# Kernel tuning notes

Hardware: AMD Instinct MI355X
Metric: run time of the kernel (lower is better)

## Reference

```python
import jax, jax.numpy as jnp
import numpy as np

B, N, D = 8, 2048, 512

def setup_inputs() -> dict:
    key = jax.random.key(0)
    k1, k2, k3, k4 = jax.random.split(key, 4)
    x = jax.random.normal(k1, (B, N, D), dtype=jnp.float32)
    x2 = jax.random.normal(k2, (B, N, D), dtype=jnp.float32)
    # nn.Linear(dim, dim): weight [D, D], bias [D]
    W = jax.random.normal(k3, (D, D), dtype=jnp.float32) * (1.0 / np.sqrt(D))
    b = jax.random.normal(k4, (D,), dtype=jnp.float32) * 0.01
    return {"x": x, "x2": x2, "W": W, "b": b}

def reference(x, x2, W, b):
    # key = softmax(x2.transpose(1,2), dim=1) -> softmax over feature axis D,
    # shape [B, D, N]; equivalently softmax(x2, axis=-1) then transpose.
    key_t = jax.nn.softmax(x2, axis=-1)          # [B, N, D], softmax over D
    query = jax.nn.softmax(x2, axis=1)            # [B, N, D], softmax over N
    # context = value @ key : [B,N,D] @ [B,D,N] -> [B,N,N]
    context = jnp.einsum('bnd,bmd->bnm', x, key_t)
    # atten = context @ query : [B,N,N] @ [B,N,D] -> [B,N,D]
    atten = jnp.einsum('bnm,bmd->bnd', context, query)
    # linear projection: atten @ W.T + b
    return jnp.einsum('bnd,ed->bne', atten, W) + b
```

## Files before the change

### kernel.cpp

```cpp
#include <hip/hip_runtime.h>


typedef __attribute__((ext_vector_type(8))) short          s16x8;
typedef __attribute__((ext_vector_type(8))) unsigned short u16x8;
typedef __attribute__((ext_vector_type(4))) float          f32x4;

#define B_ 8
#define N_ 2048
#define D_ 512

__device__ inline unsigned short f2bf(float f) {
    unsigned u = __float_as_uint(f);
    u += 0x7FFFu + ((u >> 16) & 1u);
    return (unsigned short)(u >> 16);
}

__global__ __launch_bounds__(256) void fused_sums_k(const float* __restrict__ x2,
                                                    float* __restrict__ rks,
                                                    float* __restrict__ qs) {
    __shared__ float cp[4][512];
    int w = threadIdx.x >> 6, l = threadIdx.x & 63;
    int rbase = blockIdx.x * 32;
    int b = rbase / N_;
    const int c0 = l * 8;
    float colacc[8] = {0.f, 0.f, 0.f, 0.f, 0.f, 0.f, 0.f, 0.f};
#pragma unroll
    for (int rr = 0; rr < 8; ++rr) {
        int r = rbase + w * 8 + rr;
        const float* p = x2 + (size_t)r * D_ + c0;
        float4 a = *(const float4*)p;
        float4 bb = *(const float4*)(p + 4);
        float e0 = __expf(a.x), e1 = __expf(a.y), e2 = __expf(a.z), e3 = __expf(a.w);
        float e4 = __expf(bb.x), e5 = __expf(bb.y), e6 = __expf(bb.z), e7 = __expf(bb.w);
        float s = e0 + e1 + e2 + e3 + e4 + e5 + e6 + e7;
#pragma unroll
        for (int off = 1; off < 64; off <<= 1) s += __shfl_xor(s, off);
        if (l == 0) rks[r] = 1.0f / s;
        colacc[0] += e0; colacc[1] += e1; colacc[2] += e2; colacc[3] += e3;
        colacc[4] += e4; colacc[5] += e5; colacc[6] += e6; colacc[7] += e7;
    }
#pragma unroll
    for (int c = 0; c < 8; ++c) cp[w][c0 + c] = colacc[c];
    __syncthreads();
    for (int c = threadIdx.x; c < 512; c += 256) {
        float s = cp[0][c] + cp[1][c] + cp[2][c] + cp[3][c];
        atomicAdd(&qs[b * D_ + c], s);
    }
}

__global__ __launch_bounds__(256) void softmax_tr_k(const float* __restrict__ x2,
                                                    const float* __restrict__ rks,
                                                    const float* __restrict__ qs,
                                                    unsigned short* __restrict__ Kt,
                                                    unsigned short* __restrict__ Qt) {
    __shared__ unsigned short kt[64][65], qt[64][65];
    int b = blockIdx.z, d0 = blockIdx.y * 64, m0 = blockIdx.x * 64;
    int tx = threadIdx.x & 63, w = threadIdx.x >> 6;
    float rq = 1.0f / qs[b * D_ + d0 + tx];
#pragma unroll
    for (int it = 0; it < 16; ++it) {
        int row = w * 16 + it;
        float v = x2[((size_t)b * N_ + m0 + row) * D_ + d0 + tx];
        float e = __expf(v);
        float rk = rks[b * N_ + m0 + row];
        kt[tx][row] = f2bf(e * rk);
        qt[tx][row] = f2bf(e * rq);
    }
    __syncthreads();
#pragma unroll
    for (int it = 0; it < 16; ++it) {
        int dr = w * 16 + it;
        size_t off = ((size_t)b * D_ + d0 + dr) * N_ + m0 + tx;
        Kt[off] = kt[dr][tx];
        Qt[off] = qt[dr][tx];
    }
}

__global__ __launch_bounds__(256) void cvt_bf16_k(const float* __restrict__ in,
                                                  unsigned short* __restrict__ out) {
    size_t i = ((size_t)blockIdx.x * 256 + threadIdx.x) * 8;
    float4 a = *(const float4*)(in + i);
    float4 b = *(const float4*)(in + i + 4);
    u16x8 o;
    o[0] = f2bf(a.x); o[1] = f2bf(a.y); o[2] = f2bf(a.z); o[3] = f2bf(a.w);
    o[4] = f2bf(b.x); o[5] = f2bf(b.y); o[6] = f2bf(b.z); o[7] = f2bf(b.w);
    *(u16x8*)(out + i) = o;
}

__device__ inline void gload16(const unsigned short* g, unsigned short* l) {
    __builtin_amdgcn_global_load_lds((const __attribute__((address_space(1))) void*)g,
                                     (__attribute__((address_space(3))) void*)l, 16, 0, 0);
}

template <int MODE>
__global__ __launch_bounds__(256, 4) void gemm64_k(const unsigned short* __restrict__ A,
                                                   const unsigned short* __restrict__ Bm,
                                                   void* __restrict__ Cv,
                                                   int M, int N, int K, int nsplit,
                                                   long long sA, long long sB, long long sC) {
    __shared__ unsigned short As[64 * 32], Bs[64 * 32];
    int b = blockIdx.z / nsplit, ks = blockIdx.z % nsplit;
    int klen = K / nsplit, k0 = ks * klen;
    const unsigned short* Ab = A + (size_t)b * sA;
    const unsigned short* Bb = Bm + (size_t)b * sB;
    int tid = threadIdx.x, w = tid >> 6, l = tid & 63;
    int wr = w >> 1, wc = w & 1;
    int lr = l & 15, lg = l >> 4;
    int srow = tid >> 2, scc = tid & 3;

    f32x4 acc[2][2];
#pragma unroll
    for (int i = 0; i < 2; ++i)
#pragma unroll
        for (int j = 0; j < 2; ++j) acc[i][j] = (f32x4){0.f, 0.f, 0.f, 0.f};

    const int rowbase = blockIdx.y * 64, colbase = blockIdx.x * 64;

    for (int kt = k0; kt < k0 + klen; kt += 32) {
        gload16(Ab + (size_t)(rowbase + srow) * K + kt + scc * 8, As + w * 512);
        gload16(Bb + (size_t)(colbase + srow) * K + kt + scc * 8, Bs + w * 512);
        __syncthreads();
        s16x8 af[2], bf[2];
#pragma unroll
        for (int i = 0; i < 2; ++i)
            af[i] = *(const s16x8*)&As[(wr * 32 + i * 16 + lr) * 32 + lg * 8];
#pragma unroll
        for (int j = 0; j < 2; ++j)
            bf[j] = *(const s16x8*)&Bs[(wc * 32 + j * 16 + lr) * 32 + lg * 8];
#pragma unroll
        for (int i = 0; i < 2; ++i)
#pragma unroll
            for (int j = 0; j < 2; ++j)
                acc[i][j] = __builtin_amdgcn_mfma_f32_16x16x32_bf16(af[i], bf[j], acc[i][j], 0, 0, 0);
        __syncthreads();
    }

    if (MODE == 0) {
        float* C = (float*)Cv + (size_t)b * sC;
#pragma unroll
        for (int i = 0; i < 2; ++i)
#pragma unroll
            for (int j = 0; j < 2; ++j) {
                int col = colbase + wc * 32 + j * 16 + lr;
#pragma unroll
                for (int r = 0; r < 4; ++r) {
                    int row = rowbase + wr * 32 + i * 16 + lg * 4 + r;
                    atomicAdd(&C[(size_t)row * N + col], acc[i][j][r]);
                }
            }
    } else {
        unsigned short* C = (unsigned short*)Cv + (size_t)b * sC;
#pragma unroll
        for (int i = 0; i < 2; ++i)
#pragma unroll
            for (int j = 0; j < 2; ++j) {
                int col = colbase + wc * 32 + j * 16 + lr;
#pragma unroll
                for (int r = 0; r < 4; ++r) {
                    int row = rowbase + wr * 32 + i * 16 + lg * 4 + r;
                    C[(size_t)row * N + col] = f2bf(acc[i][j][r]);
                }
            }
    }
}

__global__ __launch_bounds__(256, 2) void gemm_bt_k(const unsigned short* __restrict__ A,
                                                    const unsigned short* __restrict__ Bm,
                                                    float* __restrict__ Cv,
                                                    const float* __restrict__ bias,
                                                    int M, int N, int K,
                                                    long long sA, long long sB, long long sC) {
    __shared__ unsigned short As[128 * 32], Bs[128 * 32];
    int b = blockIdx.z;
    const unsigned short* Ab = A + (size_t)b * sA;
    const unsigned short* Bb = Bm + (size_t)b * sB;
    int tm = blockIdx.y, tn = blockIdx.x;
    int tid = threadIdx.x, w = tid >> 6, l = tid & 63;
    int wr = w >> 1, wc = w & 1;
    int lr = l & 15, lg = l >> 4;

    f32x4 acc[4][4];
#pragma unroll
    for (int i = 0; i < 4; ++i)
#pragma unroll
        for (int j = 0; j < 4; ++j) acc[i][j] = (f32x4){0.f, 0.f, 0.f, 0.f};

    const int rowbase = tm * 128, colbase = tn * 128;

    for (int kt = 0; kt < K; kt += 32) {
#pragma unroll
        for (int i = 0; i < 2; ++i) {
            int ci = (i * 4 + w) * 64 + l;
            int row = ci >> 2, cc = ci & 3;
            gload16(Ab + (size_t)(rowbase + row) * K + kt + cc * 8, As + (i * 4 + w) * 512);
            gload16(Bb + (size_t)(colbase + row) * K + kt + cc * 8, Bs + (i * 4 + w) * 512);
        }
        __syncthreads();
        s16x8 af[4], bf[4];
#pragma unroll
        for (int i = 0; i < 4; ++i)
            af[i] = *(const s16x8*)&As[(wr * 64 + i * 16 + lr) * 32 + lg * 8];
#pragma unroll
        for (int j = 0; j < 4; ++j)
            bf[j] = *(const s16x8*)&Bs[(wc * 64 + j * 16 + lr) * 32 + lg * 8];
#pragma unroll
        for (int i = 0; i < 4; ++i)
#pragma unroll
            for (int j = 0; j < 4; ++j)
                acc[i][j] = __builtin_amdgcn_mfma_f32_16x16x32_bf16(af[i], bf[j], acc[i][j], 0, 0, 0);
        __syncthreads();
    }

    float* C = Cv + (size_t)b * sC;
#pragma unroll
    for (int i = 0; i < 4; ++i)
#pragma unroll
        for (int j = 0; j < 4; ++j) {
            int col = colbase + wc * 64 + j * 16 + lr;
            float bv = bias[col];
#pragma unroll
            for (int r = 0; r < 4; ++r) {
                int row = rowbase + wr * 64 + i * 16 + lg * 4 + r;
                C[(size_t)row * N + col] = acc[i][j][r] + bv;
            }
        }
}

extern "C" void kernel_launch(void* const* d_in, const int* in_sizes, int n_in,
                              void* d_out, int out_size, void* d_ws, size_t ws_size,
                              hipStream_t stream) {
    const float* x    = (const float*)d_in[0];
    const float* x2   = (const float*)d_in[1];
    const float* W    = (const float*)d_in[2];
    const float* bias = (const float*)d_in[3];
    float* out = (float*)d_out;

    unsigned short* Kt  = (unsigned short*)d_ws;
    unsigned short* Qt  = Kt + 8388608;
    unsigned short* xb  = Qt + 8388608;
    unsigned short* Wb  = xb + 8388608;
    unsigned short* KQb = Wb + 262144;
    unsigned short* Mt  = KQb + 2097152;
    float* KQf = (float*)(Mt + 2097152);
    float* qs  = KQf + 2097152;
    float* rks = qs + 4096;

    hipMemsetAsync(KQf, 0, (2097152 + 4096) * sizeof(float), stream);

    fused_sums_k<<<dim3(B_ * N_ / 32), 256, 0, stream>>>(x2, rks, qs);

    softmax_tr_k<<<dim3(N_ / 64, D_ / 64, B_), 256, 0, stream>>>(x2, rks, qs, Kt, Qt);

    cvt_bf16_k<<<dim3(4096), 256, 0, stream>>>(x, xb);
    cvt_bf16_k<<<dim3(128), 256, 0, stream>>>(W, Wb);

    gemm64_k<0><<<dim3(8, 8, B_ * 2), 256, 0, stream>>>(
        Kt, Qt, KQf, 512, 512, 2048, 2,
        (long long)512 * 2048, (long long)512 * 2048, (long long)512 * 512);

    cvt_bf16_k<<<dim3(1024), 256, 0, stream>>>(KQf, KQb);

    gemm64_k<2><<<dim3(8, 8, B_), 256, 0, stream>>>(
        Wb, KQb, Mt, 512, 512, 512, 1,
        0LL, (long long)512 * 512, (long long)512 * 512);

    gemm_bt_k<<<dim3(4, 16, B_), 256, 0, stream>>>(
        xb, Mt, out, bias, 2048, 512, 512,
        (long long)2048 * 512, (long long)512 * 512, (long long)2048 * 512);
}
```

Baseline: 193.5 us.

## Factor softmax scales into one shared transposed matrix and fuse x conversion into GEMM

The row-softmax factor (split as sqrt of 1/rowsum) and the column-softmax denominator are factored out, so a single transposed bf16 matrix F serves both sides of the K^T Q GEMM. The column normalisation moves into the conversion kernel that also sums the two split-K partials. This replaces the atomic adds and the large memset. The final GEMM now loads fp32 x straight into LDS and converts it to bf16 in registers, which removes the separate x conversion pass. The changes halve the transposed write traffic and remove a full pass over x, at the cost of doubled LDS for the A tile and per-iteration conversion work in the last GEMM.

Measured after the change: 183.1 us. -5.4%, faster.

```diff
diff --git a/kernel.cpp b/kernel.cpp
--- a/kernel.cpp
+++ b/kernel.cpp
@@ -16,7 +16,7 @@
 }
 
 __global__ __launch_bounds__(256) void fused_sums_k(const float* __restrict__ x2,
-                                                    float* __restrict__ rks,
+                                                    float* __restrict__ rsq,
                                                     float* __restrict__ qs) {
     __shared__ float cp[4][512];
     int w = threadIdx.x >> 6, l = threadIdx.x & 63;
@@ -35,7 +35,7 @@
         float s = e0 + e1 + e2 + e3 + e4 + e5 + e6 + e7;
 #pragma unroll
         for (int off = 1; off < 64; off <<= 1) s += __shfl_xor(s, off);
-        if (l == 0) rks[r] = 1.0f / s;
+        if (l == 0) rsq[r] = sqrtf(1.0f / s);
         colacc[0] += e0; colacc[1] += e1; colacc[2] += e2; colacc[3] += e3;
         colacc[4] += e4; colacc[5] += e5; colacc[6] += e6; colacc[7] += e7;
     }
@@ -48,31 +48,26 @@
     }
 }
 
-__global__ __launch_bounds__(256) void softmax_tr_k(const float* __restrict__ x2,
-                                                    const float* __restrict__ rks,
-                                                    const float* __restrict__ qs,
-                                                    unsigned short* __restrict__ Kt,
-                                                    unsigned short* __restrict__ Qt) {
-    __shared__ unsigned short kt[64][65], qt[64][65];
-    int b = blockIdx.z, d0 = blockIdx.y * 64, m0 = blockIdx.x * 64;
+__global__ __launch_bounds__(256) void softmax_ft_k(const float* __restrict__ x2,
+                                                    const float* __restrict__ rsq,
+                                                    unsigned short* __restrict__ Ft) {
+    __shared__ unsigned short ft[64][65];
+    int b  = 7 - blockIdx.z;
+    int d0 = (7 - blockIdx.y) * 64;
+    int m0 = (31 - blockIdx.x) * 64;
     int tx = threadIdx.x & 63, w = threadIdx.x >> 6;
-    float rq = 1.0f / qs[b * D_ + d0 + tx];
 #pragma unroll
     for (int it = 0; it < 16; ++it) {
         int row = w * 16 + it;
         float v = x2[((size_t)b * N_ + m0 + row) * D_ + d0 + tx];
-        float e = __expf(v);
-        float rk = rks[b * N_ + m0 + row];
-        kt[tx][row] = f2bf(e * rk);
-        qt[tx][row] = f2bf(e * rq);
+        float sc = rsq[b * N_ + m0 + row];
+        ft[tx][row] = f2bf(__expf(v) * sc);
     }
     __syncthreads();
 #pragma unroll
     for (int it = 0; it < 16; ++it) {
         int dr = w * 16 + it;
-        size_t off = ((size_t)b * D_ + d0 + dr) * N_ + m0 + tx;
-        Kt[off] = kt[dr][tx];
-        Qt[off] = qt[dr][tx];
+        Ft[((size_t)b * D_ + d0 + dr) * N_ + m0 + tx] = ft[dr][tx];
     }
 }
 
@@ -87,7 +82,32 @@
     *(u16x8*)(out + i) = o;
 }
 
+__global__ __launch_bounds__(256) void cvt_kq_k(const float* __restrict__ P,
+                                                const float* __restrict__ qs,
+                                                unsigned short* __restrict__ KQb) {
+    size_t o = ((size_t)blockIdx.x * 256 + threadIdx.x) * 8;
+    int b = (int)(o >> 18);
+    size_t off = o & 262143;
+    int j0 = (int)(o & 511);
+    const float* p0 = P + ((size_t)b * 2) * 262144 + off;
+    const float* p1 = p0 + 262144;
+    float4 a0 = *(const float4*)p0,        a1 = *(const float4*)(p0 + 4);
+    float4 c0 = *(const float4*)p1,        c1 = *(const float4*)(p1 + 4);
+    float4 q0 = *(const float4*)(qs + b * D_ + j0);
+    float4 q1 = *(const float4*)(qs + b * D_ + j0 + 4);
+    u16x8 r;
+    r[0] = f2bf((a0.x + c0.x) / q0.x); r[1] = f2bf((a0.y + c0.y) / q0.y);
+    r[2] = f2bf((a0.z + c0.z) / q0.z); r[3] = f2bf((a0.w + c0.w) / q0.w);
+    r[4] = f2bf((a1.x + c1.x) / q1.x); r[5] = f2bf((a1.y + c1.y) / q1.y);
+    r[6] = f2bf((a1.z + c1.z) / q1.z); r[7] = f2bf((a1.w + c1.w) / q1.w);
+    *(u16x8*)(KQb + o) = r;
+}
+
 __device__ inline void gload16(const unsigned short* g, unsigned short* l) {
+    __builtin_amdgcn_global_load_lds((const __attribute__((address_space(1))) void*)g,
+                                     (__attribute__((address_space(3))) void*)l, 16, 0, 0);
+}
+__device__ inline void gload16f(const float* g, float* l) {
     __builtin_amdgcn_global_load_lds((const __attribute__((address_space(1))) void*)g,
                                      (__attribute__((address_space(3))) void*)l, 16, 0, 0);
 }
@@ -136,7 +156,7 @@
     }
 
     if (MODE == 0) {
-        float* C = (float*)Cv + (size_t)b * sC;
+        float* C = (float*)Cv + (size_t)blockIdx.z * sC;
 #pragma unroll
         for (int i = 0; i < 2; ++i)
 #pragma unroll
@@ -145,7 +165,7 @@
 #pragma unroll
                 for (int r = 0; r < 4; ++r) {
                     int row = rowbase + wr * 32 + i * 16 + lg * 4 + r;
-                    atomicAdd(&C[(size_t)row * N + col], acc[i][j][r]);
+                    C[(size_t)row * N + col] = acc[i][j][r];
                 }
             }
     } else {
@@ -164,16 +184,15 @@
     }
 }
 
-__global__ __launch_bounds__(256, 2) void gemm_bt_k(const unsigned short* __restrict__ A,
-                                                    const unsigned short* __restrict__ Bm,
-                                                    float* __restrict__ Cv,
-                                                    const float* __restrict__ bias,
-                                                    int M, int N, int K,
-                                                    long long sA, long long sB, long long sC) {
-    __shared__ unsigned short As[128 * 32], Bs[128 * 32];
+__global__ __launch_bounds__(256, 2) void gemm_xf32_k(const float* __restrict__ X,
+                                                      const unsigned short* __restrict__ Bm,
+                                                      float* __restrict__ Out,
+                                                      const float* __restrict__ bias) {
+    __shared__ float Asf[128 * 32];
+    __shared__ unsigned short Bs[128 * 32];
     int b = blockIdx.z;
-    const unsigned short* Ab = A + (size_t)b * sA;
-    const unsigned short* Bb = Bm + (size_t)b * sB;
+    const float* Ab = X + (size_t)b * ((size_t)N_ * D_);
+    const unsigned short* Bb = Bm + (size_t)b * ((size_t)D_ * D_);
     int tm = blockIdx.y, tn = blockIdx.x;
     int tid = threadIdx.x, w = tid >> 6, l = tid & 63;
     int wr = w >> 1, wc = w & 1;
@@ -187,19 +206,32 @@
 
     const int rowbase = tm * 128, colbase = tn * 128;
 
-    for (int kt = 0; kt < K; kt += 32) {
+    for (int kt = 0; kt < D_; kt += 32) {
+#pragma unroll
+        for (int i = 0; i < 4; ++i) {
+            int ci = (i * 4 + w) * 64 + l;
+            int row = ci >> 3, cc = ci & 7;
+            gload16f(Ab + (size_t)(rowbase + row) * D_ + kt + cc * 4, Asf + (i * 4 + w) * 256);
+        }
 #pragma unroll
         for (int i = 0; i < 2; ++i) {
             int ci = (i * 4 + w) * 64 + l;
             int row = ci >> 2, cc = ci & 3;
-            gload16(Ab + (size_t)(rowbase + row) * K + kt + cc * 8, As + (i * 4 + w) * 512);
-            gload16(Bb + (size_t)(colbase + row) * K + kt + cc * 8, Bs + (i * 4 + w) * 512);
+            gload16(Bb + (size_t)(colbase + row) * D_ + kt + cc * 8, Bs + (i * 4 + w) * 512);
         }
         __syncthreads();
         s16x8 af[4], bf[4];
 #pragma unroll
-        for (int i = 0; i < 4; ++i)
-            af[i] = *(const s16x8*)&As[(wr * 64 + i * 16 + lr) * 32 + lg * 8];
+        for (int i = 0; i < 4; ++i) {
+            const float* ap = &Asf[(wr * 64 + i * 16 + lr) * 32 + lg * 8];
+            f32x4 a0 = *(const f32x4*)ap, a1 = *(const f32x4*)(ap + 4);
+            s16x8 t;
+            t[0] = (short)f2bf(a0[0]); t[1] = (short)f2bf(a0[1]);
+            t[2] = (short)f2bf(a0[2]); t[3] = (short)f2bf(a0[3]);
+            t[4] = (short)f2bf(a1[0]); t[5] = (short)f2bf(a1[1]);
+            t[6] = (short)f2bf(a1[2]); t[7] = (short)f2bf(a1[3]);
+            af[i] = t;
+        }
 #pragma unroll
         for (int j = 0; j < 4; ++j)
             bf[j] = *(const s16x8*)&Bs[(wc * 64 + j * 16 + lr) * 32 + lg * 8];
@@ -211,7 +243,7 @@
         __syncthreads();
     }
 
-    float* C = Cv + (size_t)b * sC;
+    float* C = Out + (size_t)b * ((size_t)N_ * D_);
 #pragma unroll
     for (int i = 0; i < 4; ++i)
 #pragma unroll
@@ -221,7 +253,7 @@
 #pragma unroll
             for (int r = 0; r < 4; ++r) {
                 int row = rowbase + wr * 64 + i * 16 + lg * 4 + r;
-                C[(size_t)row * N + col] = acc[i][j][r] + bv;
+                C[(size_t)row * D_ + col] = acc[i][j][r] + bv;
             }
         }
 }
@@ -235,36 +267,31 @@
     const float* bias = (const float*)d_in[3];
     float* out = (float*)d_out;
 
-    unsigned short* Kt  = (unsigned short*)d_ws;
-    unsigned short* Qt  = Kt + 8388608;
-    unsigned short* xb  = Qt + 8388608;
-    unsigned short* Wb  = xb + 8388608;
+    unsigned short* Ft  = (unsigned short*)d_ws;
+    unsigned short* Wb  = Ft + 8388608;
     unsigned short* KQb = Wb + 262144;
     unsigned short* Mt  = KQb + 2097152;
-    float* KQf = (float*)(Mt + 2097152);
-    float* qs  = KQf + 2097152;
-    float* rks = qs + 4096;
-
-    hipMemsetAsync(KQf, 0, (2097152 + 4096) * sizeof(float), stream);
-
-    fused_sums_k<<<dim3(B_ * N_ / 32), 256, 0, stream>>>(x2, rks, qs);
-
-    softmax_tr_k<<<dim3(N_ / 64, D_ / 64, B_), 256, 0, stream>>>(x2, rks, qs, Kt, Qt);
-
-    cvt_bf16_k<<<dim3(4096), 256, 0, stream>>>(x, xb);
+    float* P   = (float*)(Mt + 2097152);
+    float* qs  = P + 4194304;
+    float* rsq = qs + 4096;
+
+    hipMemsetAsync(qs, 0, (size_t)B_ * D_ * sizeof(float), stream);
+
+    fused_sums_k<<<dim3(B_ * N_ / 32), 256, 0, stream>>>(x2, rsq, qs);
+
+    softmax_ft_k<<<dim3(N_ / 64, D_ / 64, B_), 256, 0, stream>>>(x2, rsq, Ft);
+
     cvt_bf16_k<<<dim3(128), 256, 0, stream>>>(W, Wb);
 
     gemm64_k<0><<<dim3(8, 8, B_ * 2), 256, 0, stream>>>(
-        Kt, Qt, KQf, 512, 512, 2048, 2,
+        Ft, Ft, P, 512, 512, 2048, 2,
         (long long)512 * 2048, (long long)512 * 2048, (long long)512 * 512);
 
-    cvt_bf16_k<<<dim3(1024), 256, 0, stream>>>(KQf, KQb);
+    cvt_kq_k<<<dim3(1024), 256, 0, stream>>>(P, qs, KQb);
 
     gemm64_k<2><<<dim3(8, 8, B_), 256, 0, stream>>>(
         Wb, KQb, Mt, 512, 512, 512, 1,
         0LL, (long long)512 * 512, (long long)512 * 512);
 
-    gemm_bt_k<<<dim3(4, 16, B_), 256, 0, stream>>>(
-        xb, Mt, out, bias, 2048, 512, 512,
-        (long long)2048 * 512, (long long)512 * 512, (long long)2048 * 512);
-}
+    gemm_xf32_k<<<dim3(4, 16, B_), 256, 0, stream>>>(x, Mt, out, bias);
+}
```
